# Kernel tuning notes

Hardware: AMD Instinct MI355X
Metric: run time of the kernel (lower is better)

## Reference

```python
import jax, jax.numpy as jnp
import numpy as np

N_HEAD = 16
N_KV_HEAD = 4
HEAD_DIM = 64
VE_CH = 12  # min(12, n_embd)


def apply_rotary_emb(x, cos, sin):
    d = x.shape[3] // 2
    x1, x2 = x[..., :d], x[..., d:]
    return jnp.concatenate([x1 * cos + x2 * sin, x1 * -sin + x2 * cos], axis=3)


def rms_norm(x):
    return x * jax.lax.rsqrt(jnp.mean(jnp.square(x), axis=-1, keepdims=True) + 1e-6)


def setup_inputs() -> dict:
    key = jax.random.key(0)
    ks = jax.random.split(key, 9)
    B, T, C = 2, 2048, 1024
    s = 0.02
    return {
        "x": jax.random.normal(ks[0], (B, T, C), jnp.float32),
        "ve": jax.random.normal(ks[1], (B, T, N_KV_HEAD * HEAD_DIM), jnp.float32),
        "cos": jax.random.normal(ks[2], (1, T, 1, HEAD_DIM // 2), jnp.float32),
        "sin": jax.random.normal(ks[3], (1, T, 1, HEAD_DIM // 2), jnp.float32),
        "Wq": jax.random.normal(ks[4], (C, C), jnp.float32) * s,
        "Wk": jax.random.normal(ks[5], (N_KV_HEAD * HEAD_DIM, C), jnp.float32) * s,
        "Wv": jax.random.normal(ks[6], (N_KV_HEAD * HEAD_DIM, C), jnp.float32) * s,
        "Wo": jax.random.normal(ks[7], (C, C), jnp.float32) * s,
        "Wg": jax.random.normal(ks[8], (N_KV_HEAD, VE_CH), jnp.float32) * s,
    }


def reference(x, ve, cos, sin, Wq, Wk, Wv, Wo, Wg):
    B, T, C = x.shape
    q = (x @ Wq.T).reshape(B, T, N_HEAD, HEAD_DIM)
    k = (x @ Wk.T).reshape(B, T, N_KV_HEAD, HEAD_DIM)
    v = (x @ Wv.T).reshape(B, T, N_KV_HEAD, HEAD_DIM)

    # value-embedding gate
    ve_r = ve.reshape(B, T, N_KV_HEAD, HEAD_DIM)
    gate = 3.0 * jax.nn.sigmoid(x[..., :VE_CH] @ Wg.T)  # [B,T,n_kv_head]
    v = v + gate[..., None] * ve_r

    q = apply_rotary_emb(q, cos, sin)
    k = apply_rotary_emb(k, cos, sin)
    q = rms_norm(q) * 1.2
    k = rms_norm(k) * 1.2

    # GQA: expand kv heads
    r = N_HEAD // N_KV_HEAD
    k = jnp.repeat(k, r, axis=2)
    v = jnp.repeat(v, r, axis=2)

    # [B,H,T,D]
    q = q.transpose(0, 2, 1, 3)
    k = k.transpose(0, 2, 1, 3)
    v = v.transpose(0, 2, 1, 3)

    scale = 1.0 / np.sqrt(HEAD_DIM).astype(np.float32)
    scores = jnp.einsum("bhqd,bhkd->bhqk", q, k) * scale
    causal = jnp.tril(jnp.ones((T, T), dtype=bool))
    scores = jnp.where(causal, scores, jnp.float32(-jnp.inf))
    att = jax.nn.softmax(scores, axis=-1)
    y = jnp.einsum("bhqk,bhkd->bhqd", att, v)
    y = y.transpose(0, 2, 1, 3).reshape(B, T, C)
    return y @ Wo.T
```

## Files before the change

### kernel.cpp

```cpp
#include <hip/hip_runtime.h>
#include <stdint.h>

#define B_SZ 2
#define T_SZ 2048
#define C_SZ 1024
#define NH   16
#define NKV  4
#define HD   64
#define KVD  256
#define QKV_N 1536

typedef __attribute__((ext_vector_type(8))) short bf16x8;
typedef __attribute__((ext_vector_type(4))) float f32x4;

#define GL(p) ((const __attribute__((address_space(1))) void*)(p))
#define LD(p) ((__attribute__((address_space(3))) void*)(p))

__device__ inline unsigned short f2bf(float f) {
  union { float f; unsigned u; } v; v.f = f;
  unsigned u = v.u;
  unsigned r = (u + 0x7fffu + ((u >> 16) & 1u)) >> 16;
  return (unsigned short)r;
}
__device__ inline unsigned short bftrunc(float f) {
  union { float f; unsigned u; } v; v.f = f;
  return (unsigned short)(v.u >> 16);
}

struct CvtArgs {
  const float *s0, *s1, *s2, *s3, *s4;
  unsigned short *d0, *d1, *d2, *d3, *d4;
  const float *x, *Wg;
  float *gate;
};
__global__ __launch_bounds__(256) void cvt_all(CvtArgs a) {
  int blk = blockIdx.x, tid = threadIdx.x;
  if (blk >= 6656) {
    int idx = (blk - 6656) * 256 + tid;
    int bt = idx >> 2, kh = idx & 3;
    float s = 0.f;
#pragma unroll
    for (int j = 0; j < 12; j++) s += a.x[(size_t)bt * C_SZ + j] * a.Wg[kh * 12 + j];
    a.gate[idx] = 3.f / (1.f + __expf(-s));
    return;
  }
  const float* s; unsigned short* d; int i;
  if      (blk < 4096) { s = a.s0; d = a.d0; i = blk * 256 + tid; }
  else if (blk < 5120) { s = a.s1; d = a.d1; i = (blk - 4096) * 256 + tid; }
  else if (blk < 5376) { s = a.s2; d = a.d2; i = (blk - 5120) * 256 + tid; }
  else if (blk < 5632) { s = a.s3; d = a.d3; i = (blk - 5376) * 256 + tid; }
  else                 { s = a.s4; d = a.d4; i = (blk - 5632) * 256 + tid; }
  float4 f = ((const float4*)s)[i];
  ushort4 o;
  o.x = f2bf(f.x); o.y = f2bf(f.y); o.z = f2bf(f.z); o.w = f2bf(f.w);
  ((ushort4*)d)[i] = o;
}

#define BM 64
#define BN 128
#define GEMM_PROLOG(A, Bm, K)                                                        \
  __shared__ unsigned short As[2][BM * 32];                                          \
  __shared__ unsigned short Bs[2][BN * 32];                                          \
  int tid  = threadIdx.x;                                                            \
  int lane = tid & 63;                                                               \
  int wave = tid >> 6;                                                               \
  int quad = lane >> 4;                                                              \
  int l16  = lane & 15;                                                              \
  int m0 = blockIdx.y * BM;                                                          \
  int n0 = blockIdx.x * BN;                                                          \
  int wm = (wave & 1) * 32;                                                          \
  int wn = (wave >> 1) * 64;                                                         \
  f32x4 acc[2][4];                                                                   \
  _Pragma("unroll") for (int i = 0; i < 2; i++)                                      \
    _Pragma("unroll") for (int j = 0; j < 4; j++)                                    \
      acc[i][j] = (f32x4){0.f, 0.f, 0.f, 0.f};                                       \
  int lrow = lane >> 2;                                                              \
  int lcol = (lane & 3) * 8;                                                         \
  int srowA = wave * 16;                                                             \
  int srowB = wave * 32;                                                             \
  const unsigned short* aP  = &A[(size_t)(m0 + srowA + lrow) * K + lcol];            \
  const unsigned short* b0P = &Bm[(size_t)(n0 + srowB + lrow) * K + lcol];           \
  const unsigned short* b1P = b0P + 16 * (size_t)K;                                  \
  for (int k0 = 0; k0 < K; k0 += 64) {                                               \
    __syncthreads();                                                                 \
    _Pragma("unroll") for (int p = 0; p < 2; p++) {                                  \
      __builtin_amdgcn_global_load_lds(GL(aP  + k0 + p * 32), LD(&As[p][srowA * 32]), 16, 0, 0); \
      __builtin_amdgcn_global_load_lds(GL(b0P + k0 + p * 32), LD(&Bs[p][srowB * 32]), 16, 0, 0); \
      __builtin_amdgcn_global_load_lds(GL(b1P + k0 + p * 32), LD(&Bs[p][(srowB + 16) * 32]), 16, 0, 0); \
    }                                                                                \
    __syncthreads();                                                                 \
    _Pragma("unroll") for (int p = 0; p < 2; p++) {                                  \
      bf16x8 af[2], bfr[4];                                                          \
      _Pragma("unroll") for (int i = 0; i < 2; i++)                                  \
        af[i] = *(const bf16x8*)&As[p][(wm + i * 16 + l16) * 32 + quad * 8];         \
      _Pragma("unroll") for (int j = 0; j < 4; j++)                                  \
        bfr[j] = *(const bf16x8*)&Bs[p][(wn + j * 16 + l16) * 32 + quad * 8];        \
      _Pragma("unroll") for (int i = 0; i < 2; i++)                                  \
        _Pragma("unroll") for (int j = 0; j < 4; j++)                                \
          acc[i][j] = __builtin_amdgcn_mfma_f32_16x16x32_bf16(af[i], bfr[j], acc[i][j], 0, 0, 0); \
    }                                                                                \
  }

__global__ __launch_bounds__(256) void gemm_bt(const unsigned short* __restrict__ A,
                                               const unsigned short* __restrict__ Bm,
                                               float* __restrict__ C,
                                               int N, int K) {
  GEMM_PROLOG(A, Bm, K)
#pragma unroll
  for (int i = 0; i < 2; i++) {
#pragma unroll
    for (int j = 0; j < 4; j++) {
      int col = n0 + wn + j * 16 + l16;
#pragma unroll
      for (int r = 0; r < 4; r++) {
        int row = m0 + wm + i * 16 + quad * 4 + r;
        C[(size_t)row * N + col] = acc[i][j][r];
      }
    }
  }
}

__global__ __launch_bounds__(256) void gemm_qkv(const unsigned short* __restrict__ A,
                                                const unsigned short* __restrict__ Bm,
                                                const float* __restrict__ ve,
                                                const float* __restrict__ cosb,
                                                const float* __restrict__ sinb,
                                                const float* __restrict__ gateArr,
                                                unsigned short* __restrict__ qa,
                                                unsigned short* __restrict__ ka,
                                                unsigned short* __restrict__ vt) {
  const int K = C_SZ;
  GEMM_PROLOG(A, Bm, K)

  int colbase = n0 + wn;
  if (colbase < 1280) {
    int isQ = colbase < 1024;
    int h   = isQ ? (colbase >> 6) : ((colbase - 1024) >> 6);
    float scale = isQ ? (0.15f * 1.44269504088896f) : 1.2f;
    unsigned short* dst = isQ ? qa : ka;
    int nheads = isQ ? NH : NKV;
#pragma unroll
    for (int i = 0; i < 2; i++) {
#pragma unroll
      for (int r = 0; r < 4; r++) {
        int row = m0 + wm + i * 16 + quad * 4 + r;
        int t = row & (T_SZ - 1), b = row >> 11;
        float a10 = acc[i][0][r], a11 = acc[i][1][r];
        float a20 = acc[i][2][r], a21 = acc[i][3][r];
        float cv0 = cosb[t * 32 + l16],      sv0 = sinb[t * 32 + l16];
        float cv1 = cosb[t * 32 + 16 + l16], sv1 = sinb[t * 32 + 16 + l16];
        float o10 =  a10 * cv0 + a20 * sv0;
        float o11 =  a11 * cv1 + a21 * sv1;
        float o20 = -a10 * sv0 + a20 * cv0;
        float o21 = -a11 * sv1 + a21 * cv1;
        float ssq = o10 * o10 + o11 * o11 + o20 * o20 + o21 * o21;
        ssq += __shfl_xor(ssq, 1);
        ssq += __shfl_xor(ssq, 2);
        ssq += __shfl_xor(ssq, 4);
        ssq += __shfl_xor(ssq, 8);
        float rn = rsqrtf(ssq * (1.f / 64.f) + 1e-6f) * scale;
        size_t base = ((size_t)(b * nheads + h) * T_SZ + t) * HD;
        dst[base + l16]      = f2bf(o10 * rn);
        dst[base + 16 + l16] = f2bf(o11 * rn);
        dst[base + 32 + l16] = f2bf(o20 * rn);
        dst[base + 48 + l16] = f2bf(o21 * rn);
      }
    }
  } else {
    int kh = (colbase - 1280) >> 6;
#pragma unroll
    for (int i = 0; i < 2; i++) {
#pragma unroll
      for (int r = 0; r < 4; r++) {
        int row = m0 + wm + i * 16 + quad * 4 + r;
        int t = row & (T_SZ - 1), b = row >> 11;
        float g = gateArr[row * 4 + kh];
        size_t vbase = ((size_t)(b * NKV + kh) * HD) * T_SZ;
#pragma unroll
        for (int j = 0; j < 4; j++) {
          int d = j * 16 + l16;
          float val = acc[i][j][r] + g * ve[(size_t)row * KVD + kh * HD + d];
          vt[vbase + (size_t)d * T_SZ + t] = f2bf(val);
        }
      }
    }
  }
}

#define KSTR 72
__global__ __launch_bounds__(256) void attn(const unsigned short* __restrict__ qa,
                                            const unsigned short* __restrict__ ka,
                                            const unsigned short* __restrict__ vt,
                                            unsigned short* __restrict__ y) {
  int bid = blockIdx.x;
  int half = bid >> 8, r = bid & 255;
  int qt = half ? (r & 15) : 15 - (r & 15);
  int bh = (half << 4) | (r >> 4);
  int b = bh >> 4, h = bh & 15;
  int kh = h >> 2;
  int tid = threadIdx.x;
  int wave = tid >> 6, lane = tid & 63;
  int quad = lane >> 4, l16 = lane & 15;

  __shared__ unsigned short Ks[64 * KSTR];
  __shared__ unsigned short Vs[64 * KSTR];
  __shared__ unsigned short Ps[128 * KSTR];
  unsigned short* Pw = &Ps[(wave * 32) * KSTR];

  bf16x8 aq[2][2];
#pragma unroll
  for (int mi = 0; mi < 2; mi++) {
    int tq = qt * 128 + wave * 32 + mi * 16 + l16;
    const unsigned short* qp = &qa[((size_t)(b * NH + h) * T_SZ + tq) * HD];
    aq[mi][0] = *(const bf16x8*)&qp[quad * 8];
    aq[mi][1] = *(const bf16x8*)&qp[32 + quad * 8];
  }

  const unsigned short one_bf = 0x3F80;
  bf16x8 vones = {(short)one_bf, (short)one_bf, (short)one_bf, (short)one_bf,
                  (short)one_bf, (short)one_bf, (short)one_bf, (short)one_bf};

  f32x4 oacc[2][4];
  f32x4 lacc[2];
#pragma unroll
  for (int mi = 0; mi < 2; mi++) {
    lacc[mi] = (f32x4){0.f, 0.f, 0.f, 0.f};
#pragma unroll
    for (int d = 0; d < 4; d++) oacc[mi][d] = (f32x4){0.f, 0.f, 0.f, 0.f};
  }

  int lr = tid >> 2;
  int lc = (tid & 3) * 16;

  const unsigned short* kbase = &ka[(size_t)(b * NKV + kh) * T_SZ * HD];
  const unsigned short* vbase = &vt[(size_t)(b * NKV + kh) * HD * T_SZ];

  int nj = 2 * qt + 2;

  uint4 k0, k1, v0, v1;
  {
    const unsigned short* kp = &kbase[(size_t)lr * HD + lc];
    const unsigned short* vp = &vbase[(size_t)lr * T_SZ + lc];
    k0 = *(const uint4*)(kp);
    k1 = *(const uint4*)(kp + 8);
    v0 = *(const uint4*)(vp);
    v1 = *(const uint4*)(vp + 8);
  }

  int qrow0 = qt * 128 + wave * 32;

  for (int j = 0; j < nj; j++) {
    __syncthreads();
    *(uint4*)&Ks[lr * KSTR + lc]     = k0;
    *(uint4*)&Ks[lr * KSTR + lc + 8] = k1;
    *(uint4*)&Vs[lr * KSTR + lc]     = v0;
    *(uint4*)&Vs[lr * KSTR + lc + 8] = v1;
    if (j + 1 < nj) {
      const unsigned short* kp = &kbase[(size_t)((j + 1) * 64 + lr) * HD + lc];
      const unsigned short* vp = &vbase[(size_t)lr * T_SZ + (j + 1) * 64 + lc];
      k0 = *(const uint4*)(kp);
      k1 = *(const uint4*)(kp + 8);
      v0 = *(const uint4*)(vp);
      v1 = *(const uint4*)(vp + 8);
    }
    __syncthreads();

    f32x4 sa[2][4];
#pragma unroll
    for (int nb = 0; nb < 4; nb++) {
      bf16x8 bk0 = *(const bf16x8*)&Ks[(nb * 16 + l16) * KSTR + quad * 8];
      bf16x8 bk1 = *(const bf16x8*)&Ks[(nb * 16 + l16) * KSTR + 32 + quad * 8];
#pragma unroll
      for (int mi = 0; mi < 2; mi++) {
        f32x4 s = (f32x4){0.f, 0.f, 0.f, 0.f};
        s = __builtin_amdgcn_mfma_f32_16x16x32_bf16(aq[mi][0], bk0, s, 0, 0, 0);
        s = __builtin_amdgcn_mfma_f32_16x16x32_bf16(aq[mi][1], bk1, s, 0, 0, 0);
        sa[mi][nb] = s;
      }
    }

#pragma unroll
    for (int mi = 0; mi < 2; mi++) {
      int rowLow = qrow0 + mi * 16;
      if (j * 64 + 63 > rowLow) {
#pragma unroll
        for (int nb = 0; nb < 4; nb++) {
          int col = j * 64 + nb * 16 + l16;
#pragma unroll
          for (int i = 0; i < 4; i++) {
            if (col > rowLow + quad * 4 + i) sa[mi][nb][i] = -__builtin_inff();
          }
        }
      }
    }

#pragma unroll
    for (int mi = 0; mi < 2; mi++)
#pragma unroll
      for (int nb = 0; nb < 4; nb++)
#pragma unroll
        for (int i = 0; i < 4; i++)
          Pw[(mi * 16 + quad * 4 + i) * KSTR + nb * 16 + l16] =
              bftrunc(__builtin_amdgcn_exp2f(sa[mi][nb][i]));

    bf16x8 ap[2][2];
#pragma unroll
    for (int mi = 0; mi < 2; mi++) {
      ap[mi][0] = *(const bf16x8*)&Pw[(mi * 16 + l16) * KSTR + quad * 8];
      ap[mi][1] = *(const bf16x8*)&Pw[(mi * 16 + l16) * KSTR + 32 + quad * 8];
      lacc[mi] = __builtin_amdgcn_mfma_f32_16x16x32_bf16(ap[mi][0], vones, lacc[mi], 0, 0, 0);
      lacc[mi] = __builtin_amdgcn_mfma_f32_16x16x32_bf16(ap[mi][1], vones, lacc[mi], 0, 0, 0);
    }
#pragma unroll
    for (int d = 0; d < 4; d++) {
      bf16x8 bv0 = *(const bf16x8*)&Vs[(d * 16 + l16) * KSTR + quad * 8];
      bf16x8 bv1 = *(const bf16x8*)&Vs[(d * 16 + l16) * KSTR + 32 + quad * 8];
#pragma unroll
      for (int mi = 0; mi < 2; mi++) {
        oacc[mi][d] = __builtin_amdgcn_mfma_f32_16x16x32_bf16(ap[mi][0], bv0, oacc[mi][d], 0, 0, 0);
        oacc[mi][d] = __builtin_amdgcn_mfma_f32_16x16x32_bf16(ap[mi][1], bv1, oacc[mi][d], 0, 0, 0);
      }
    }
  }

#pragma unroll
  for (int mi = 0; mi < 2; mi++) {
#pragma unroll
    for (int i = 0; i < 4; i++) {
      int tq = qrow0 + mi * 16 + quad * 4 + i;
      float inv = 1.f / lacc[mi][i];
#pragma unroll
      for (int d = 0; d < 4; d++) {
        y[((size_t)(b * T_SZ) + tq) * C_SZ + h * HD + d * 16 + l16] = f2bf(oacc[mi][d][i] * inv);
      }
    }
  }
}

extern "C" void kernel_launch(void* const* d_in, const int* in_sizes, int n_in,
                              void* d_out, int out_size, void* d_ws, size_t ws_size,
                              hipStream_t stream) {
  const float* x    = (const float*)d_in[0];
  const float* ve   = (const float*)d_in[1];
  const float* cosb = (const float*)d_in[2];
  const float* sinb = (const float*)d_in[3];
  const float* Wq   = (const float*)d_in[4];
  const float* Wk   = (const float*)d_in[5];
  const float* Wv   = (const float*)d_in[6];
  const float* Wo   = (const float*)d_in[7];
  const float* Wg   = (const float*)d_in[8];
  float* out = (float*)d_out;

  const size_t MB = 1024 * 1024;
  char* ws = (char*)d_ws;
  unsigned short* xb    = (unsigned short*)(ws);
  unsigned short* wqkvb = (unsigned short*)(ws + 8 * MB);
  unsigned short* wob   = (unsigned short*)(ws + 11 * MB);
  unsigned short* qab   = (unsigned short*)(ws + 13 * MB);
  unsigned short* kab   = (unsigned short*)(ws + 21 * MB);
  unsigned short* vtb   = (unsigned short*)(ws + 23 * MB);
  float*          gateA = (float*)(ws + 25 * MB);
  unsigned short* yb    = xb;

  CvtArgs ca;
  ca.s0 = x;  ca.d0 = xb;
  ca.s1 = Wq; ca.d1 = wqkvb;
  ca.s2 = Wk; ca.d2 = wqkvb + 1024 * 1024;
  ca.s3 = Wv; ca.d3 = wqkvb + 1280 * 1024;
  ca.s4 = Wo; ca.d4 = wob;
  ca.x = x; ca.Wg = Wg; ca.gate = gateA;
  cvt_all<<<6720, 256, 0, stream>>>(ca);

  gemm_qkv<<<dim3(QKV_N / BN, (B_SZ * T_SZ) / BM), 256, 0, stream>>>(
      xb, wqkvb, ve, cosb, sinb, gateA, qab, kab, vtb);

  attn<<<512, 256, 0, stream>>>(qab, kab, vtb, yb);

  gemm_bt<<<dim3(C_SZ / BN, (B_SZ * T_SZ) / BM), 256, 0, stream>>>(
      yb, wob, out, C_SZ, C_SZ);
}
```

Before: 179.8 us.

## Enlarge GEMM tiles to 128x128 and attention KV blocks to 128 keys

The shared GEMM prologue moves from 64x128 to 128x128 tiles, so each wave now accumulates a 64x64 sub-tile with 16 MFMA accumulators. This raises reuse of each staged operand but halves the grid, to 192 and 256 blocks. The attention kernel now stages 128 keys per iteration instead of 64, halving loop trips and barriers and applying the causal mask only on the diagonal block. The cost is more LDS, more register pressure, and more wasted masked work in the diagonal block.

```diff
diff --git a/kernel.cpp b/kernel.cpp
--- a/kernel.cpp
+++ b/kernel.cpp
@@ -56,46 +56,43 @@
   ((ushort4*)d)[i] = o;
 }
 
-#define BM 64
-#define BN 128
 #define GEMM_PROLOG(A, Bm, K)                                                        \
-  __shared__ unsigned short As[2][BM * 32];                                          \
-  __shared__ unsigned short Bs[2][BN * 32];                                          \
+  __shared__ unsigned short As[2][128 * 32];                                         \
+  __shared__ unsigned short Bs[2][128 * 32];                                         \
   int tid  = threadIdx.x;                                                            \
   int lane = tid & 63;                                                               \
   int wave = tid >> 6;                                                               \
   int quad = lane >> 4;                                                              \
   int l16  = lane & 15;                                                              \
-  int m0 = blockIdx.y * BM;                                                          \
-  int n0 = blockIdx.x * BN;                                                          \
-  int wm = (wave & 1) * 32;                                                          \
+  int m0 = blockIdx.y * 128;                                                         \
+  int n0 = blockIdx.x * 128;                                                         \
+  int wm = (wave & 1) * 64;                                                          \
   int wn = (wave >> 1) * 64;                                                         \
-  f32x4 acc[2][4];                                                                   \
-  _Pragma("unroll") for (int i = 0; i < 2; i++)                                      \
+  f32x4 acc[4][4];                                                                   \
+  _Pragma("unroll") for (int i = 0; i < 4; i++)                                      \
     _Pragma("unroll") for (int j = 0; j < 4; j++)                                    \
       acc[i][j] = (f32x4){0.f, 0.f, 0.f, 0.f};                                       \
   int lrow = lane >> 2;                                                              \
   int lcol = (lane & 3) * 8;                                                         \
-  int srowA = wave * 16;                                                             \
-  int srowB = wave * 32;                                                             \
-  const unsigned short* aP  = &A[(size_t)(m0 + srowA + lrow) * K + lcol];            \
-  const unsigned short* b0P = &Bm[(size_t)(n0 + srowB + lrow) * K + lcol];           \
-  const unsigned short* b1P = b0P + 16 * (size_t)K;                                  \
+  int srow = wave * 32;                                                              \
+  const unsigned short* aP = &A[(size_t)(m0 + srow + lrow) * K + lcol];              \
+  const unsigned short* bP = &Bm[(size_t)(n0 + srow + lrow) * K + lcol];             \
   for (int k0 = 0; k0 < K; k0 += 64) {                                               \
     __syncthreads();                                                                 \
     _Pragma("unroll") for (int p = 0; p < 2; p++) {                                  \
-      __builtin_amdgcn_global_load_lds(GL(aP  + k0 + p * 32), LD(&As[p][srowA * 32]), 16, 0, 0); \
-      __builtin_amdgcn_global_load_lds(GL(b0P + k0 + p * 32), LD(&Bs[p][srowB * 32]), 16, 0, 0); \
-      __builtin_amdgcn_global_load_lds(GL(b1P + k0 + p * 32), LD(&Bs[p][(srowB + 16) * 32]), 16, 0, 0); \
+      __builtin_amdgcn_global_load_lds(GL(aP + k0 + p * 32),          LD(&As[p][srow * 32]),        16, 0, 0); \
+      __builtin_amdgcn_global_load_lds(GL(aP + 16 * (size_t)K + k0 + p * 32), LD(&As[p][(srow + 16) * 32]), 16, 0, 0); \
+      __builtin_amdgcn_global_load_lds(GL(bP + k0 + p * 32),          LD(&Bs[p][srow * 32]),        16, 0, 0); \
+      __builtin_amdgcn_global_load_lds(GL(bP + 16 * (size_t)K + k0 + p * 32), LD(&Bs[p][(srow + 16) * 32]), 16, 0, 0); \
     }                                                                                \
     __syncthreads();                                                                 \
     _Pragma("unroll") for (int p = 0; p < 2; p++) {                                  \
-      bf16x8 af[2], bfr[4];                                                          \
-      _Pragma("unroll") for (int i = 0; i < 2; i++)                                  \
+      bf16x8 af[4], bfr[4];                                                          \
+      _Pragma("unroll") for (int i = 0; i < 4; i++)                                  \
         af[i] = *(const bf16x8*)&As[p][(wm + i * 16 + l16) * 32 + quad * 8];         \
       _Pragma("unroll") for (int j = 0; j < 4; j++)                                  \
         bfr[j] = *(const bf16x8*)&Bs[p][(wn + j * 16 + l16) * 32 + quad * 8];        \
-      _Pragma("unroll") for (int i = 0; i < 2; i++)                                  \
+      _Pragma("unroll") for (int i = 0; i < 4; i++)                                  \
         _Pragma("unroll") for (int j = 0; j < 4; j++)                                \
           acc[i][j] = __builtin_amdgcn_mfma_f32_16x16x32_bf16(af[i], bfr[j], acc[i][j], 0, 0, 0); \
     }                                                                                \
@@ -107,7 +104,7 @@
                                                int N, int K) {
   GEMM_PROLOG(A, Bm, K)
 #pragma unroll
-  for (int i = 0; i < 2; i++) {
+  for (int i = 0; i < 4; i++) {
 #pragma unroll
     for (int j = 0; j < 4; j++) {
       int col = n0 + wn + j * 16 + l16;
@@ -140,7 +137,7 @@
     unsigned short* dst = isQ ? qa : ka;
     int nheads = isQ ? NH : NKV;
 #pragma unroll
-    for (int i = 0; i < 2; i++) {
+    for (int i = 0; i < 4; i++) {
 #pragma unroll
       for (int r = 0; r < 4; r++) {
         int row = m0 + wm + i * 16 + quad * 4 + r;
@@ -169,7 +166,7 @@
   } else {
     int kh = (colbase - 1280) >> 6;
 #pragma unroll
-    for (int i = 0; i < 2; i++) {
+    for (int i = 0; i < 4; i++) {
 #pragma unroll
       for (int r = 0; r < 4; r++) {
         int row = m0 + wm + i * 16 + quad * 4 + r;
@@ -187,7 +184,8 @@
   }
 }
 
-#define KSTR 72
+#define KST 72
+#define VST 136
 __global__ __launch_bounds__(256) void attn(const unsigned short* __restrict__ qa,
                                             const unsigned short* __restrict__ ka,
                                             const unsigned short* __restrict__ vt,
@@ -202,10 +200,10 @@
   int wave = tid >> 6, lane = tid & 63;
   int quad = lane >> 4, l16 = lane & 15;
 
-  __shared__ unsigned short Ks[64 * KSTR];
-  __shared__ unsigned short Vs[64 * KSTR];
-  __shared__ unsigned short Ps[128 * KSTR];
-  unsigned short* Pw = &Ps[(wave * 32) * KSTR];
+  __shared__ unsigned short Ks[128 * KST];
+  __shared__ unsigned short Vs[64 * VST];
+  __shared__ unsigned short Ps[128 * VST];
+  unsigned short* Pw = &Ps[(wave * 32) * VST];
 
   bf16x8 aq[2][2];
 #pragma unroll
@@ -229,47 +227,45 @@
     for (int d = 0; d < 4; d++) oacc[mi][d] = (f32x4){0.f, 0.f, 0.f, 0.f};
   }
 
-  int lr = tid >> 2;
-  int lc = (tid & 3) * 16;
+  int klr = tid >> 1, klc = (tid & 1) * 32;
+  int vlr = tid >> 2, vlc = (tid & 3) * 32;
 
   const unsigned short* kbase = &ka[(size_t)(b * NKV + kh) * T_SZ * HD];
   const unsigned short* vbase = &vt[(size_t)(b * NKV + kh) * HD * T_SZ];
 
-  int nj = 2 * qt + 2;
-
-  uint4 k0, k1, v0, v1;
+  int nj = qt + 1;
+
+  uint4 kr[4], vr[4];
   {
-    const unsigned short* kp = &kbase[(size_t)lr * HD + lc];
-    const unsigned short* vp = &vbase[(size_t)lr * T_SZ + lc];
-    k0 = *(const uint4*)(kp);
-    k1 = *(const uint4*)(kp + 8);
-    v0 = *(const uint4*)(vp);
-    v1 = *(const uint4*)(vp + 8);
+    const unsigned short* kp = &kbase[(size_t)klr * HD + klc];
+    const unsigned short* vp = &vbase[(size_t)vlr * T_SZ + vlc];
+#pragma unroll
+    for (int q = 0; q < 4; q++) { kr[q] = *(const uint4*)(kp + q * 8); vr[q] = *(const uint4*)(vp + q * 8); }
   }
 
   int qrow0 = qt * 128 + wave * 32;
 
   for (int j = 0; j < nj; j++) {
     __syncthreads();
-    *(uint4*)&Ks[lr * KSTR + lc]     = k0;
-    *(uint4*)&Ks[lr * KSTR + lc + 8] = k1;
-    *(uint4*)&Vs[lr * KSTR + lc]     = v0;
-    *(uint4*)&Vs[lr * KSTR + lc + 8] = v1;
+#pragma unroll
+    for (int q = 0; q < 4; q++) {
+      *(uint4*)&Ks[klr * KST + klc + q * 8] = kr[q];
+      *(uint4*)&Vs[vlr * VST + vlc + q * 8] = vr[q];
+    }
+    __syncthreads();
+
     if (j + 1 < nj) {
-      const unsigned short* kp = &kbase[(size_t)((j + 1) * 64 + lr) * HD + lc];
-      const unsigned short* vp = &vbase[(size_t)lr * T_SZ + (j + 1) * 64 + lc];
-      k0 = *(const uint4*)(kp);
-      k1 = *(const uint4*)(kp + 8);
-      v0 = *(const uint4*)(vp);
-      v1 = *(const uint4*)(vp + 8);
-    }
-    __syncthreads();
-
-    f32x4 sa[2][4];
-#pragma unroll
-    for (int nb = 0; nb < 4; nb++) {
-      bf16x8 bk0 = *(const bf16x8*)&Ks[(nb * 16 + l16) * KSTR + quad * 8];
-      bf16x8 bk1 = *(const bf16x8*)&Ks[(nb * 16 + l16) * KSTR + 32 + quad * 8];
+      const unsigned short* kp = &kbase[(size_t)((j + 1) * 128 + klr) * HD + klc];
+      const unsigned short* vp = &vbase[(size_t)vlr * T_SZ + (j + 1) * 128 + vlc];
+#pragma unroll
+      for (int q = 0; q < 4; q++) { kr[q] = *(const uint4*)(kp + q * 8); vr[q] = *(const uint4*)(vp + q * 8); }
+    }
+
+    f32x4 sa[2][8];
+#pragma unroll
+    for (int nb = 0; nb < 8; nb++) {
+      bf16x8 bk0 = *(const bf16x8*)&Ks[(nb * 16 + l16) * KST + quad * 8];
+      bf16x8 bk1 = *(const bf16x8*)&Ks[(nb * 16 + l16) * KST + 32 + quad * 8];
 #pragma unroll
       for (int mi = 0; mi < 2; mi++) {
         f32x4 s = (f32x4){0.f, 0.f, 0.f, 0.f};
@@ -279,13 +275,13 @@
       }
     }
 
-#pragma unroll
-    for (int mi = 0; mi < 2; mi++) {
-      int rowLow = qrow0 + mi * 16;
-      if (j * 64 + 63 > rowLow) {
-#pragma unroll
-        for (int nb = 0; nb < 4; nb++) {
-          int col = j * 64 + nb * 16 + l16;
+    if (j == qt) {
+#pragma unroll
+      for (int mi = 0; mi < 2; mi++) {
+        int rowLow = qrow0 + mi * 16;
+#pragma unroll
+        for (int nb = 0; nb < 8; nb++) {
+          int col = j * 128 + nb * 16 + l16;
 #pragma unroll
           for (int i = 0; i < 4; i++) {
             if (col > rowLow + quad * 4 + i) sa[mi][nb][i] = -__builtin_inff();
@@ -297,28 +293,29 @@
 #pragma unroll
     for (int mi = 0; mi < 2; mi++)
 #pragma unroll
-      for (int nb = 0; nb < 4; nb++)
+      for (int nb = 0; nb < 8; nb++)
 #pragma unroll
         for (int i = 0; i < 4; i++)
-          Pw[(mi * 16 + quad * 4 + i) * KSTR + nb * 16 + l16] =
+          Pw[(mi * 16 + quad * 4 + i) * VST + nb * 16 + l16] =
               bftrunc(__builtin_amdgcn_exp2f(sa[mi][nb][i]));
 
-    bf16x8 ap[2][2];
+    bf16x8 ap[2][4];
 #pragma unroll
     for (int mi = 0; mi < 2; mi++) {
-      ap[mi][0] = *(const bf16x8*)&Pw[(mi * 16 + l16) * KSTR + quad * 8];
-      ap[mi][1] = *(const bf16x8*)&Pw[(mi * 16 + l16) * KSTR + 32 + quad * 8];
-      lacc[mi] = __builtin_amdgcn_mfma_f32_16x16x32_bf16(ap[mi][0], vones, lacc[mi], 0, 0, 0);
-      lacc[mi] = __builtin_amdgcn_mfma_f32_16x16x32_bf16(ap[mi][1], vones, lacc[mi], 0, 0, 0);
-    }
-#pragma unroll
-    for (int d = 0; d < 4; d++) {
-      bf16x8 bv0 = *(const bf16x8*)&Vs[(d * 16 + l16) * KSTR + quad * 8];
-      bf16x8 bv1 = *(const bf16x8*)&Vs[(d * 16 + l16) * KSTR + 32 + quad * 8];
-#pragma unroll
-      for (int mi = 0; mi < 2; mi++) {
-        oacc[mi][d] = __builtin_amdgcn_mfma_f32_16x16x32_bf16(ap[mi][0], bv0, oacc[mi][d], 0, 0, 0);
-        oacc[mi][d] = __builtin_amdgcn_mfma_f32_16x16x32_bf16(ap[mi][1], bv1, oacc[mi][d], 0, 0, 0);
+#pragma unroll
+      for (int c = 0; c < 4; c++) {
+        ap[mi][c] = *(const bf16x8*)&Pw[(mi * 16 + l16) * VST + c * 32 + quad * 8];
+        lacc[mi] = __builtin_amdgcn_mfma_f32_16x16x32_bf16(ap[mi][c], vones, lacc[mi], 0, 0, 0);
+      }
+    }
+#pragma unroll
+    for (int c = 0; c < 4; c++) {
+#pragma unroll
+      for (int d = 0; d < 4; d++) {
+        bf16x8 bv = *(const bf16x8*)&Vs[(d * 16 + l16) * VST + c * 32 + quad * 8];
+#pragma unroll
+        for (int mi = 0; mi < 2; mi++)
+          oacc[mi][d] = __builtin_amdgcn_mfma_f32_16x16x32_bf16(ap[mi][c], bv, oacc[mi][d], 0, 0, 0);
       }
     }
   }
@@ -371,11 +368,11 @@
   ca.x = x; ca.Wg = Wg; ca.gate = gateA;
   cvt_all<<<6720, 256, 0, stream>>>(ca);
 
-  gemm_qkv<<<dim3(QKV_N / BN, (B_SZ * T_SZ) / BM), 256, 0, stream>>>(
+  gemm_qkv<<<dim3(QKV_N / 128, (B_SZ * T_SZ) / 128), 256, 0, stream>>>(
       xb, wqkvb, ve, cosb, sinb, gateA, qab, kab, vtb);
 
   attn<<<512, 256, 0, stream>>>(qab, kab, vtb, yb);
 
-  gemm_bt<<<dim3(C_SZ / BN, (B_SZ * T_SZ) / BM), 256, 0, stream>>>(
+  gemm_bt<<<dim3(C_SZ / 128, (B_SZ * T_SZ) / 128), 256, 0, stream>>>(
       yb, wob, out, C_SZ, C_SZ);
 }
```

Result: slower. 214.3 us (+19.2%).

## Deepen GEMM K-step to 128 and transpose attention score MFMA for vector P stores

Applied to the files above, without the earlier changes.

The shared GEMM prologue now stages 128 K-elements per iteration (four 32-wide LDS slabs) instead of 64, halving the number of barrier pairs per tile at the cost of doubled LDS usage. In attention, the QK^T MFMA operands are swapped so each lane holds four consecutive key positions for one query, letting P be written to LDS as one ushort4 per block instead of scattered scalar stores. The K/V LDS write barrier is moved ahead of the next-tile global prefetch. More LDS per GEMM block may reduce occupancy.

```diff
diff --git a/kernel.cpp b/kernel.cpp
--- a/kernel.cpp
+++ b/kernel.cpp
@@ -56,18 +56,16 @@
   ((ushort4*)d)[i] = o;
 }
 
-#define BM 64
-#define BN 128
 #define GEMM_PROLOG(A, Bm, K)                                                        \
-  __shared__ unsigned short As[2][BM * 32];                                          \
-  __shared__ unsigned short Bs[2][BN * 32];                                          \
+  __shared__ unsigned short As[4][64 * 32];                                          \
+  __shared__ unsigned short Bs[4][128 * 32];                                         \
   int tid  = threadIdx.x;                                                            \
   int lane = tid & 63;                                                               \
   int wave = tid >> 6;                                                               \
   int quad = lane >> 4;                                                              \
   int l16  = lane & 15;                                                              \
-  int m0 = blockIdx.y * BM;                                                          \
-  int n0 = blockIdx.x * BN;                                                          \
+  int m0 = blockIdx.y * 64;                                                          \
+  int n0 = blockIdx.x * 128;                                                         \
   int wm = (wave & 1) * 32;                                                          \
   int wn = (wave >> 1) * 64;                                                         \
   f32x4 acc[2][4];                                                                   \
@@ -81,15 +79,15 @@
   const unsigned short* aP  = &A[(size_t)(m0 + srowA + lrow) * K + lcol];            \
   const unsigned short* b0P = &Bm[(size_t)(n0 + srowB + lrow) * K + lcol];           \
   const unsigned short* b1P = b0P + 16 * (size_t)K;                                  \
-  for (int k0 = 0; k0 < K; k0 += 64) {                                               \
+  for (int k0 = 0; k0 < K; k0 += 128) {                                              \
     __syncthreads();                                                                 \
-    _Pragma("unroll") for (int p = 0; p < 2; p++) {                                  \
-      __builtin_amdgcn_global_load_lds(GL(aP  + k0 + p * 32), LD(&As[p][srowA * 32]), 16, 0, 0); \
-      __builtin_amdgcn_global_load_lds(GL(b0P + k0 + p * 32), LD(&Bs[p][srowB * 32]), 16, 0, 0); \
+    _Pragma("unroll") for (int p = 0; p < 4; p++) {                                  \
+      __builtin_amdgcn_global_load_lds(GL(aP  + k0 + p * 32), LD(&As[p][srowA * 32]),        16, 0, 0); \
+      __builtin_amdgcn_global_load_lds(GL(b0P + k0 + p * 32), LD(&Bs[p][srowB * 32]),        16, 0, 0); \
       __builtin_amdgcn_global_load_lds(GL(b1P + k0 + p * 32), LD(&Bs[p][(srowB + 16) * 32]), 16, 0, 0); \
     }                                                                                \
     __syncthreads();                                                                 \
-    _Pragma("unroll") for (int p = 0; p < 2; p++) {                                  \
+    _Pragma("unroll") for (int p = 0; p < 4; p++) {                                  \
       bf16x8 af[2], bfr[4];                                                          \
       _Pragma("unroll") for (int i = 0; i < 2; i++)                                  \
         af[i] = *(const bf16x8*)&As[p][(wm + i * 16 + l16) * 32 + quad * 8];         \
@@ -187,7 +185,8 @@
   }
 }
 
-#define KSTR 72
+#define KST 72
+#define PST 72
 __global__ __launch_bounds__(256) void attn(const unsigned short* __restrict__ qa,
                                             const unsigned short* __restrict__ ka,
                                             const unsigned short* __restrict__ vt,
@@ -202,18 +201,18 @@
   int wave = tid >> 6, lane = tid & 63;
   int quad = lane >> 4, l16 = lane & 15;
 
-  __shared__ unsigned short Ks[64 * KSTR];
-  __shared__ unsigned short Vs[64 * KSTR];
-  __shared__ unsigned short Ps[128 * KSTR];
-  unsigned short* Pw = &Ps[(wave * 32) * KSTR];
-
-  bf16x8 aq[2][2];
-#pragma unroll
-  for (int mi = 0; mi < 2; mi++) {
-    int tq = qt * 128 + wave * 32 + mi * 16 + l16;
+  __shared__ unsigned short Ks[64 * KST];
+  __shared__ unsigned short Vs[64 * KST];
+  __shared__ unsigned short Ps[128 * PST];
+  unsigned short* Pw = &Ps[(wave * 32) * PST];
+
+  bf16x8 bq[2][2];
+#pragma unroll
+  for (int qi = 0; qi < 2; qi++) {
+    int tq = qt * 128 + wave * 32 + qi * 16 + l16;
     const unsigned short* qp = &qa[((size_t)(b * NH + h) * T_SZ + tq) * HD];
-    aq[mi][0] = *(const bf16x8*)&qp[quad * 8];
-    aq[mi][1] = *(const bf16x8*)&qp[32 + quad * 8];
+    bq[qi][0] = *(const bf16x8*)&qp[quad * 8];
+    bq[qi][1] = *(const bf16x8*)&qp[32 + quad * 8];
   }
 
   const unsigned short one_bf = 0x3F80;
@@ -223,10 +222,10 @@
   f32x4 oacc[2][4];
   f32x4 lacc[2];
 #pragma unroll
-  for (int mi = 0; mi < 2; mi++) {
-    lacc[mi] = (f32x4){0.f, 0.f, 0.f, 0.f};
-#pragma unroll
-    for (int d = 0; d < 4; d++) oacc[mi][d] = (f32x4){0.f, 0.f, 0.f, 0.f};
+  for (int qi = 0; qi < 2; qi++) {
+    lacc[qi] = (f32x4){0.f, 0.f, 0.f, 0.f};
+#pragma unroll
+    for (int d = 0; d < 4; d++) oacc[qi][d] = (f32x4){0.f, 0.f, 0.f, 0.f};
   }
 
   int lr = tid >> 2;
@@ -251,10 +250,12 @@
 
   for (int j = 0; j < nj; j++) {
     __syncthreads();
-    *(uint4*)&Ks[lr * KSTR + lc]     = k0;
-    *(uint4*)&Ks[lr * KSTR + lc + 8] = k1;
-    *(uint4*)&Vs[lr * KSTR + lc]     = v0;
-    *(uint4*)&Vs[lr * KSTR + lc + 8] = v1;
+    *(uint4*)&Ks[lr * KST + lc]     = k0;
+    *(uint4*)&Ks[lr * KST + lc + 8] = k1;
+    *(uint4*)&Vs[lr * KST + lc]     = v0;
+    *(uint4*)&Vs[lr * KST + lc + 8] = v1;
+    __syncthreads();
+
     if (j + 1 < nj) {
       const unsigned short* kp = &kbase[(size_t)((j + 1) * 64 + lr) * HD + lc];
       const unsigned short* vp = &vbase[(size_t)lr * T_SZ + (j + 1) * 64 + lc];
@@ -263,75 +264,75 @@
       v0 = *(const uint4*)(vp);
       v1 = *(const uint4*)(vp + 8);
     }
-    __syncthreads();
-
-    f32x4 sa[2][4];
-#pragma unroll
-    for (int nb = 0; nb < 4; nb++) {
-      bf16x8 bk0 = *(const bf16x8*)&Ks[(nb * 16 + l16) * KSTR + quad * 8];
-      bf16x8 bk1 = *(const bf16x8*)&Ks[(nb * 16 + l16) * KSTR + 32 + quad * 8];
-#pragma unroll
-      for (int mi = 0; mi < 2; mi++) {
+
+    f32x4 st[4][2];
+#pragma unroll
+    for (int tb = 0; tb < 4; tb++) {
+      bf16x8 ak0 = *(const bf16x8*)&Ks[(tb * 16 + l16) * KST + quad * 8];
+      bf16x8 ak1 = *(const bf16x8*)&Ks[(tb * 16 + l16) * KST + 32 + quad * 8];
+#pragma unroll
+      for (int qi = 0; qi < 2; qi++) {
         f32x4 s = (f32x4){0.f, 0.f, 0.f, 0.f};
-        s = __builtin_amdgcn_mfma_f32_16x16x32_bf16(aq[mi][0], bk0, s, 0, 0, 0);
-        s = __builtin_amdgcn_mfma_f32_16x16x32_bf16(aq[mi][1], bk1, s, 0, 0, 0);
-        sa[mi][nb] = s;
-      }
-    }
-
-#pragma unroll
-    for (int mi = 0; mi < 2; mi++) {
-      int rowLow = qrow0 + mi * 16;
-      if (j * 64 + 63 > rowLow) {
-#pragma unroll
-        for (int nb = 0; nb < 4; nb++) {
-          int col = j * 64 + nb * 16 + l16;
+        s = __builtin_amdgcn_mfma_f32_16x16x32_bf16(ak0, bq[qi][0], s, 0, 0, 0);
+        s = __builtin_amdgcn_mfma_f32_16x16x32_bf16(ak1, bq[qi][1], s, 0, 0, 0);
+        st[tb][qi] = s;
+      }
+    }
+
+#pragma unroll
+    for (int qi = 0; qi < 2; qi++) {
+      int qlow = qrow0 + qi * 16;
+      if (j * 64 + 63 > qlow) {
+        int qg = qlow + l16;
+#pragma unroll
+        for (int tb = 0; tb < 4; tb++) {
+          int tg = j * 64 + tb * 16 + quad * 4;
 #pragma unroll
           for (int i = 0; i < 4; i++) {
-            if (col > rowLow + quad * 4 + i) sa[mi][nb][i] = -__builtin_inff();
+            if (tg + i > qg) st[tb][qi][i] = -__builtin_inff();
           }
         }
       }
-    }
-
-#pragma unroll
-    for (int mi = 0; mi < 2; mi++)
-#pragma unroll
-      for (int nb = 0; nb < 4; nb++)
-#pragma unroll
-        for (int i = 0; i < 4; i++)
-          Pw[(mi * 16 + quad * 4 + i) * KSTR + nb * 16 + l16] =
-              bftrunc(__builtin_amdgcn_exp2f(sa[mi][nb][i]));
+#pragma unroll
+      for (int tb = 0; tb < 4; tb++) {
+        ushort4 w;
+        w.x = bftrunc(__builtin_amdgcn_exp2f(st[tb][qi][0]));
+        w.y = bftrunc(__builtin_amdgcn_exp2f(st[tb][qi][1]));
+        w.z = bftrunc(__builtin_amdgcn_exp2f(st[tb][qi][2]));
+        w.w = bftrunc(__builtin_amdgcn_exp2f(st[tb][qi][3]));
+        *(ushort4*)&Pw[(qi * 16 + l16) * PST + tb * 16 + quad * 4] = w;
+      }
+    }
 
     bf16x8 ap[2][2];
 #pragma unroll
-    for (int mi = 0; mi < 2; mi++) {
-      ap[mi][0] = *(const bf16x8*)&Pw[(mi * 16 + l16) * KSTR + quad * 8];
-      ap[mi][1] = *(const bf16x8*)&Pw[(mi * 16 + l16) * KSTR + 32 + quad * 8];
-      lacc[mi] = __builtin_amdgcn_mfma_f32_16x16x32_bf16(ap[mi][0], vones, lacc[mi], 0, 0, 0);
-      lacc[mi] = __builtin_amdgcn_mfma_f32_16x16x32_bf16(ap[mi][1], vones, lacc[mi], 0, 0, 0);
+    for (int qi = 0; qi < 2; qi++) {
+      ap[qi][0] = *(const bf16x8*)&Pw[(qi * 16 + l16) * PST + quad * 8];
+      ap[qi][1] = *(const bf16x8*)&Pw[(qi * 16 + l16) * PST + 32 + quad * 8];
+      lacc[qi] = __builtin_amdgcn_mfma_f32_16x16x32_bf16(ap[qi][0], vones, lacc[qi], 0, 0, 0);
+      lacc[qi] = __builtin_amdgcn_mfma_f32_16x16x32_bf16(ap[qi][1], vones, lacc[qi], 0, 0, 0);
     }
 #pragma unroll
     for (int d = 0; d < 4; d++) {
-      bf16x8 bv0 = *(const bf16x8*)&Vs[(d * 16 + l16) * KSTR + quad * 8];
-      bf16x8 bv1 = *(const bf16x8*)&Vs[(d * 16 + l16) * KSTR + 32 + quad * 8];
-#pragma unroll
-      for (int mi = 0; mi < 2; mi++) {
-        oacc[mi][d] = __builtin_amdgcn_mfma_f32_16x16x32_bf16(ap[mi][0], bv0, oacc[mi][d], 0, 0, 0);
-        oacc[mi][d] = __builtin_amdgcn_mfma_f32_16x16x32_bf16(ap[mi][1], bv1, oacc[mi][d], 0, 0, 0);
-      }
-    }
-  }
-
-#pragma unroll
-  for (int mi = 0; mi < 2; mi++) {
+      bf16x8 bv0 = *(const bf16x8*)&Vs[(d * 16 + l16) * KST + quad * 8];
+      bf16x8 bv1 = *(const bf16x8*)&Vs[(d * 16 + l16) * KST + 32 + quad * 8];
+#pragma unroll
+      for (int qi = 0; qi < 2; qi++) {
+        oacc[qi][d] = __builtin_amdgcn_mfma_f32_16x16x32_bf16(ap[qi][0], bv0, oacc[qi][d], 0, 0, 0);
+        oacc[qi][d] = __builtin_amdgcn_mfma_f32_16x16x32_bf16(ap[qi][1], bv1, oacc[qi][d], 0, 0, 0);
+      }
+    }
+  }
+
+#pragma unroll
+  for (int qi = 0; qi < 2; qi++) {
 #pragma unroll
     for (int i = 0; i < 4; i++) {
-      int tq = qrow0 + mi * 16 + quad * 4 + i;
-      float inv = 1.f / lacc[mi][i];
+      int tq = qrow0 + qi * 16 + quad * 4 + i;
+      float inv = 1.f / lacc[qi][i];
 #pragma unroll
       for (int d = 0; d < 4; d++) {
-        y[((size_t)(b * T_SZ) + tq) * C_SZ + h * HD + d * 16 + l16] = f2bf(oacc[mi][d][i] * inv);
+        y[((size_t)(b * T_SZ) + tq) * C_SZ + h * HD + d * 16 + l16] = f2bf(oacc[qi][d][i] * inv);
       }
     }
   }
@@ -371,11 +372,11 @@
   ca.x = x; ca.Wg = Wg; ca.gate = gateA;
   cvt_all<<<6720, 256, 0, stream>>>(ca);
 
-  gemm_qkv<<<dim3(QKV_N / BN, (B_SZ * T_SZ) / BM), 256, 0, stream>>>(
+  gemm_qkv<<<dim3(QKV_N / 128, (B_SZ * T_SZ) / 64), 256, 0, stream>>>(
       xb, wqkvb, ve, cosb, sinb, gateA, qab, kab, vtb);
 
   attn<<<512, 256, 0, stream>>>(qab, kab, vtb, yb);
 
-  gemm_bt<<<dim3(C_SZ / BN, (B_SZ * T_SZ) / BM), 256, 0, stream>>>(
+  gemm_bt<<<dim3(C_SZ / 128, (B_SZ * T_SZ) / 64), 256, 0, stream>>>(
       yb, wob, out, C_SZ, C_SZ);
 }
```

After: 172.0 us. 4.3% less time.
